# Kernel optimization log

Hardware: AMD Instinct MI355X
Metric: run time of the kernel (lower is better)

Reference implementation:

```python
import jax, jax.numpy as jnp
import numpy as np

N, VW, DW, VP, DP, H, M = 1024, 50000, 300, 50, 100, 512, 256


def _run_dir(x, Wih, Whh, b, reverse):
    # Single-direction LSTM over [n, in] -> [n, H]. PyTorch gate order i,f,g,o.
    Hh = Whh.shape[1]
    def step(carry, xt):
        h, c = carry
        z = xt @ Wih.T + h @ Whh.T + b  # [4H]
        i, f, g, o = jnp.split(z, 4, axis=-1)
        c = jax.nn.sigmoid(f) * c + jax.nn.sigmoid(i) * jnp.tanh(g)
        h = jax.nn.sigmoid(o) * jnp.tanh(c)
        return (h, c), h
    init = (jnp.zeros((Hh,), x.dtype), jnp.zeros((Hh,), x.dtype))
    _, hs = jax.lax.scan(step, init, x, reverse=reverse)
    return hs


def setup_inputs() -> dict:
    key = jax.random.key(0)
    ks = jax.random.split(key, 24)
    s = 0.05  # small init to keep tanh/sigmoid unsaturated
    d = {
        "word_idx": jax.random.randint(ks[0], (N,), 0, VW, dtype=jnp.int32),
        "pos_idx": jax.random.randint(ks[1], (N,), 0, VP, dtype=jnp.int32),
        "word_emb": jax.random.normal(ks[2], (VW, DW), jnp.float32) * s,
        "pos_emb": jax.random.normal(ks[3], (VP, DP), jnp.float32) * s,
        "wih0f": jax.random.normal(ks[4], (4 * H, DW + DP), jnp.float32) * s,
        "whh0f": jax.random.normal(ks[5], (4 * H, H), jnp.float32) * s,
        "b0f": jax.random.normal(ks[6], (4 * H,), jnp.float32) * s,
        "wih0r": jax.random.normal(ks[7], (4 * H, DW + DP), jnp.float32) * s,
        "whh0r": jax.random.normal(ks[8], (4 * H, H), jnp.float32) * s,
        "b0r": jax.random.normal(ks[9], (4 * H,), jnp.float32) * s,
        "wih1f": jax.random.normal(ks[10], (4 * H, 2 * H), jnp.float32) * s,
        "whh1f": jax.random.normal(ks[11], (4 * H, H), jnp.float32) * s,
        "b1f": jax.random.normal(ks[12], (4 * H,), jnp.float32) * s,
        "wih1r": jax.random.normal(ks[13], (4 * H, 2 * H), jnp.float32) * s,
        "whh1r": jax.random.normal(ks[14], (4 * H, H), jnp.float32) * s,
        "b1r": jax.random.normal(ks[15], (4 * H,), jnp.float32) * s,
        "W1": jax.random.normal(ks[16], (M, 4 * H), jnp.float32) * s,
        "bmlp1": jax.random.normal(ks[17], (M,), jnp.float32) * s,
        "w2": jax.random.normal(ks[18], (1, M), jnp.float32) * s,
        "b2": jax.random.normal(ks[19], (1,), jnp.float32) * s,
    }
    return d


def reference(word_idx, pos_idx, word_emb, pos_emb,
              wih0f, whh0f, b0f, wih0r, whh0r, b0r,
              wih1f, whh1f, b1f, wih1r, whh1r, b1r,
              W1, bmlp1, w2, b2):
    # Embed words + pos, concat -> [n, 400]
    x = jnp.concatenate([word_emb[word_idx], pos_emb[pos_idx]], axis=1)
    # 2-layer bidirectional LSTM encoder (batch of 1 squeezed away, as in the module)
    h0 = jnp.concatenate([_run_dir(x, wih0f, whh0f, b0f, False),
                          _run_dir(x, wih0r, whh0r, b0r, True)], axis=1)   # [n, 2H]
    h1 = jnp.concatenate([_run_dir(h0, wih1f, whh1f, b1f, False),
                          _run_dir(h0, wih1r, whh1r, b1r, True)], axis=1)  # [n, 2H]
    # Pairwise MLP score: MLP(concat(h_i, h_j)). Split W1 into head/dep halves so the
    # big GEMM is done once per token instead of once per pair (same math).
    twoH = h1.shape[1]
    a = h1 @ W1[:, :twoH].T            # [n, M], contribution of h_i
    bpart = h1 @ W1[:, twoH:].T        # [n, M], contribution of h_j
    hidden = jnp.tanh(a[:, None, :] + bpart[None, :, :] + bmlp1)  # [n, n, M]
    scores = hidden @ w2[0] + b2[0]    # [n, n]
    return scores
```

## Files before the change

kernel.cpp:

```cpp
#include <hip/hip_runtime.h>
#include <hip/hip_bf16.h>

#define HID   512
#define SEQ   1024
#define GATES 2048

__device__ __forceinline__ float sigm(float x) {
    return 1.f / (1.f + __expf(-x));
}
__device__ __forceinline__ float tanh_fast(float x) {
    float ax = fabsf(x);
    float e  = __expf(-2.f * ax);
    float t  = (1.f - e) * __builtin_amdgcn_rcpf(1.f + e);
    return copysignf(t, x);
}
__device__ __forceinline__ float bcast(float v, int l) {
    return __uint_as_float((unsigned)__builtin_amdgcn_readlane((int)__float_as_uint(v), l));
}

__global__ void embed_kernel(const int* __restrict__ wi, const int* __restrict__ pi,
                             const float* __restrict__ we, const float* __restrict__ pe,
                             float* __restrict__ x) {
    int i = blockIdx.x;
    int t = threadIdx.x;
    const float* w = we + (size_t)wi[i] * 300;
    const float* p = pe + (size_t)pi[i] * 100;
    float* xo = x + (size_t)i * 400;
    for (int c = t; c < 300; c += 128) xo[c]       = w[c];
    for (int c = t; c < 100; c += 128) xo[300 + c] = p[c];
}

__global__ __launch_bounds__(256)
void gemm_bias2(const float* __restrict__ A,
                const float* __restrict__ B0, const float* __restrict__ bias0, float* __restrict__ C0,
                const float* __restrict__ B1, const float* __restrict__ bias1, float* __restrict__ C1,
                int M, int N, int K, int lda, int ldb, int ldc) {
    const float* B    = blockIdx.z ? B1    : B0;
    const float* bias = blockIdx.z ? bias1 : bias0;
    float*       C    = blockIdx.z ? C1    : C0;

    __shared__ __align__(16) float As[16 * 132];
    __shared__ __align__(16) float Bs[16 * 68];
    const int tid  = threadIdx.x;
    const int bn   = blockIdx.x, bm = blockIdx.y;
    const int tj   = tid & 15, ti = tid >> 4;
    const int arow = tid >> 1;
    const int ak8  = (tid & 1) * 8;
    const int brow = tid >> 2;
    const int bk4  = (tid & 3) * 4;
    float acc[8][4] = {};

    for (int kt = 0; kt < K; kt += 16) {
        float4 a0 = *(const float4*)(A + (size_t)(bm * 128 + arow) * lda + kt + ak8);
        float4 a1 = *(const float4*)(A + (size_t)(bm * 128 + arow) * lda + kt + ak8 + 4);
        float4 bv = *(const float4*)(B + (size_t)(bn * 64 + brow) * ldb + kt + bk4);
        As[(ak8 + 0) * 132 + arow] = a0.x; As[(ak8 + 1) * 132 + arow] = a0.y;
        As[(ak8 + 2) * 132 + arow] = a0.z; As[(ak8 + 3) * 132 + arow] = a0.w;
        As[(ak8 + 4) * 132 + arow] = a1.x; As[(ak8 + 5) * 132 + arow] = a1.y;
        As[(ak8 + 6) * 132 + arow] = a1.z; As[(ak8 + 7) * 132 + arow] = a1.w;
        Bs[(bk4 + 0) * 68 + brow] = bv.x; Bs[(bk4 + 1) * 68 + brow] = bv.y;
        Bs[(bk4 + 2) * 68 + brow] = bv.z; Bs[(bk4 + 3) * 68 + brow] = bv.w;
        __syncthreads();
        #pragma unroll
        for (int k = 0; k < 16; ++k) {
            float4 x0 = *(const float4*)&As[k * 132 + ti * 8];
            float4 x1 = *(const float4*)&As[k * 132 + ti * 8 + 4];
            float4 b4 = *(const float4*)&Bs[k * 68 + tj * 4];
            const float av[8] = {x0.x, x0.y, x0.z, x0.w, x1.x, x1.y, x1.z, x1.w};
            #pragma unroll
            for (int i = 0; i < 8; ++i) {
                acc[i][0] = fmaf(av[i], b4.x, acc[i][0]);
                acc[i][1] = fmaf(av[i], b4.y, acc[i][1]);
                acc[i][2] = fmaf(av[i], b4.z, acc[i][2]);
                acc[i][3] = fmaf(av[i], b4.w, acc[i][3]);
            }
        }
        __syncthreads();
    }
    const int n0 = bn * 64 + tj * 4;
    float bb0 = 0.f, bb1 = 0.f, bb2 = 0.f, bb3 = 0.f;
    if (bias) { bb0 = bias[n0]; bb1 = bias[n0 + 1]; bb2 = bias[n0 + 2]; bb3 = bias[n0 + 3]; }
    #pragma unroll
    for (int i = 0; i < 8; ++i) {
        float4 o;
        o.x = acc[i][0] + bb0; o.y = acc[i][1] + bb1;
        o.z = acc[i][2] + bb2; o.w = acc[i][3] + bb3;
        *(float4*)(C + (size_t)(bm * 128 + ti * 8 + i) * ldc + n0) = o;
    }
}

__global__ __launch_bounds__(512)
void lstm_layer(const float* __restrict__ Zf, const float* __restrict__ Zr,
                const float* __restrict__ WhhF, const float* __restrict__ WhhR,
                unsigned long long* __restrict__ Hpair,
                float* __restrict__ Hout,
                unsigned tagBase) {
    const int dir = blockIdx.x >> 5;
    const int wg  = blockIdx.x & 31;
    const float* __restrict__ Z   = dir ? Zr   : Zf;
    const float* __restrict__ Whh = dir ? WhhR : WhhF;
    const int colOff = dir ? HID : 0;

    const int tid  = threadIdx.x;
    const int wave = tid >> 6;
    const int lane = tid & 63;
    const int g    = lane >> 4;
    const int jj   = lane & 15;
    const int grow = g * HID + wg * 16 + jj;

    float w[64];
    {
        const float4* wp = (const float4*)(Whh + (size_t)grow * HID + wave * 64);
        #pragma unroll
        for (int q = 0; q < 16; ++q) {
            float4 v = wp[q];
            w[4 * q] = v.x; w[4 * q + 1] = v.y; w[4 * q + 2] = v.z; w[4 * q + 3] = v.w;
        }
    }

    __shared__ float part[2][8 * 65];
    float cval = 0.f;

    for (int s = 0; s < SEQ; ++s) {
        const int t = dir ? (SEQ - 1 - s) : s;

        float zin = 0.f;
        if (wave == 0) zin = Z[(size_t)t * GATES + grow];

        float acc = 0.f;
        if (s > 0) {
            const int tp = dir ? (t + 1) : (t - 1);
            const unsigned expTag = tagBase + (unsigned)s - 1u;
            const unsigned long long* hp = Hpair + (size_t)tp * (2 * HID) + colOff + wave * 64;
            unsigned long long v;
            for (;;) {
                v = __hip_atomic_load(hp + lane, __ATOMIC_RELAXED, __HIP_MEMORY_SCOPE_AGENT);
                if (__all((unsigned)(v >> 32) == expTag)) break;
            }
            float hv = __uint_as_float((unsigned)v);
            float a0 = 0.f, a1 = 0.f, a2 = 0.f, a3 = 0.f;
            #pragma unroll
            for (int m = 0; m < 64; m += 4) {
                a0 = fmaf(w[m + 0], bcast(hv, m + 0), a0);
                a1 = fmaf(w[m + 1], bcast(hv, m + 1), a1);
                a2 = fmaf(w[m + 2], bcast(hv, m + 2), a2);
                a3 = fmaf(w[m + 3], bcast(hv, m + 3), a3);
            }
            acc = (a0 + a1) + (a2 + a3);
        }
        part[s & 1][wave * 65 + lane] = acc;
        __syncthreads();

        if (wave == 0) {
            const float* pp = part[s & 1];
            float r = zin;
            #pragma unroll
            for (int c = 0; c < 8; ++c) r += pp[c * 65 + lane];
            float nl = (g == 2) ? tanh_fast(r) : sigm(r);
            float ig = __shfl(nl, jj);
            float fg = __shfl(nl, 16 + jj);
            float gg = __shfl(nl, 32 + jj);
            float og = __shfl(nl, 48 + jj);
            if (lane < 16) {
                cval = fg * cval + ig * gg;
                float hv = og * tanh_fast(cval);
                const size_t oidx = (size_t)t * (2 * HID) + colOff + wg * 16 + lane;
                unsigned long long pk = ((unsigned long long)(tagBase + (unsigned)s) << 32)
                                      | (unsigned long long)__float_as_uint(hv);
                __hip_atomic_store(Hpair + oidx, pk, __ATOMIC_RELAXED, __HIP_MEMORY_SCOPE_AGENT);
                Hout[oidx] = hv;
            }
        }
    }
}

__global__ __launch_bounds__(256)
void pairwise_kernel(const float* __restrict__ Ah, const float* __restrict__ Bd,
                     const float* __restrict__ w2, const float* __restrict__ b2,
                     float* __restrict__ out) {
    __shared__ __align__(16) float at[16 * 260];
    __shared__ __align__(16) float bt[16 * 260];
    __shared__ __align__(16) float wl[256];
    const int tid = threadIdx.x;
    const int i0 = blockIdx.y * 16, j0 = blockIdx.x * 16;
    for (int u = tid; u < 16 * 256; u += 256) {
        int r = u >> 8, m = u & 255;
        at[r * 260 + m] = Ah[(size_t)(i0 + r) * 256 + m];
        bt[r * 260 + m] = Bd[(size_t)(j0 + r) * 256 + m];
    }
    wl[tid] = w2[tid];
    __syncthreads();
    const int tj = tid & 15, ti = tid >> 4;
    float acc = b2[0];
    #pragma unroll 2
    for (int m = 0; m < 256; m += 4) {
        float4 a4 = *(const float4*)&at[ti * 260 + m];
        float4 b4 = *(const float4*)&bt[tj * 260 + m];
        float4 w4 = *(const float4*)&wl[m];
        acc += tanh_fast(a4.x + b4.x) * w4.x;
        acc += tanh_fast(a4.y + b4.y) * w4.y;
        acc += tanh_fast(a4.z + b4.z) * w4.z;
        acc += tanh_fast(a4.w + b4.w) * w4.w;
    }
    out[(size_t)(i0 + ti) * 1024 + (j0 + tj)] = acc;
}

extern "C" void kernel_launch(void* const* d_in, const int* in_sizes, int n_in,
                              void* d_out, int out_size, void* d_ws, size_t ws_size,
                              hipStream_t stream) {
    const int*   wi    = (const int*)  d_in[0];
    const int*   pi    = (const int*)  d_in[1];
    const float* we    = (const float*)d_in[2];
    const float* pe    = (const float*)d_in[3];
    const float* wih0f = (const float*)d_in[4];
    const float* whh0f = (const float*)d_in[5];
    const float* b0f   = (const float*)d_in[6];
    const float* wih0r = (const float*)d_in[7];
    const float* whh0r = (const float*)d_in[8];
    const float* b0r   = (const float*)d_in[9];
    const float* wih1f = (const float*)d_in[10];
    const float* whh1f = (const float*)d_in[11];
    const float* b1f   = (const float*)d_in[12];
    const float* wih1r = (const float*)d_in[13];
    const float* whh1r = (const float*)d_in[14];
    const float* b1r   = (const float*)d_in[15];
    const float* W1    = (const float*)d_in[16];
    const float* bmlp1 = (const float*)d_in[17];
    const float* w2    = (const float*)d_in[18];
    const float* b2    = (const float*)d_in[19];
    float* out = (float*)d_out;

    char* wsb = (char*)d_ws;
    float* x  = (float*)(wsb + 512);
    float* zA = x  + (size_t)1024 * 400;
    float* zB = zA + (size_t)1024 * 2048;
    float* h0 = zB + (size_t)1024 * 2048;
    float* h1 = h0 + (size_t)1024 * 1024;
    float* aH = h1 + (size_t)1024 * 1024;
    float* bD = aH + (size_t)1024 * 256;
    unsigned long long* Hpair = (unsigned long long*)(bD + (size_t)1024 * 256);

    embed_kernel<<<dim3(1024), dim3(128), 0, stream>>>(wi, pi, we, pe, x);

    gemm_bias2<<<dim3(32, 8, 2), dim3(256), 0, stream>>>(
        x, wih0f, b0f, zA, wih0r, b0r, zB, 1024, 2048, 400, 400, 400, 2048);

    lstm_layer<<<dim3(64), dim3(512), 0, stream>>>(zA, zB, whh0f, whh0r, Hpair, h0, 1u);

    gemm_bias2<<<dim3(32, 8, 2), dim3(256), 0, stream>>>(
        h0, wih1f, b1f, zA, wih1r, b1r, zB, 1024, 2048, 1024, 1024, 1024, 2048);

    lstm_layer<<<dim3(64), dim3(512), 0, stream>>>(zA, zB, whh1f, whh1r, Hpair, h1, 8192u);

    gemm_bias2<<<dim3(4, 8, 2), dim3(256), 0, stream>>>(
        h1, W1, bmlp1, aH, W1 + 1024, nullptr, bD, 1024, 256, 1024, 1024, 2048, 256);

    pairwise_kernel<<<dim3(64, 64), dim3(256), 0, stream>>>(aH, bD, w2, b2, out);
}
```

Measured before the change: 3.464 ms.

## Specialize LSTM waves into gate wave and matvec waves with Z prefetch

The recurrent LSTM kernel now launches 576 threads per block. Wave 0 only reduces the partial sums, applies the gate nonlinearities and publishes h. The other eight waves hold the Whh slices in registers and do the polled h·Whh matvec. Wave 0 prefetches the next timestep's input-projection row so that global load is off the per-step critical path. The polling loop alternates two outstanding atomic loads to cut spin latency. The cost is one extra wave per block, and correctness now relies on the two roles hitting the same number of barriers per step.

```diff
diff --git a/kernel.cpp b/kernel.cpp
--- a/kernel.cpp
+++ b/kernel.cpp
@@ -89,7 +89,7 @@
     }
 }
 
-__global__ __launch_bounds__(512)
+__global__ __launch_bounds__(576)
 void lstm_layer(const float* __restrict__ Zf, const float* __restrict__ Zr,
                 const float* __restrict__ WhhF, const float* __restrict__ WhhR,
                 unsigned long long* __restrict__ Hpair,
@@ -108,50 +108,19 @@
     const int jj   = lane & 15;
     const int grow = g * HID + wg * 16 + jj;
 
-    float w[64];
-    {
-        const float4* wp = (const float4*)(Whh + (size_t)grow * HID + wave * 64);
-        #pragma unroll
-        for (int q = 0; q < 16; ++q) {
-            float4 v = wp[q];
-            w[4 * q] = v.x; w[4 * q + 1] = v.y; w[4 * q + 2] = v.z; w[4 * q + 3] = v.w;
-        }
-    }
-
     __shared__ float part[2][8 * 65];
-    float cval = 0.f;
-
-    for (int s = 0; s < SEQ; ++s) {
-        const int t = dir ? (SEQ - 1 - s) : s;
-
-        float zin = 0.f;
-        if (wave == 0) zin = Z[(size_t)t * GATES + grow];
-
-        float acc = 0.f;
-        if (s > 0) {
-            const int tp = dir ? (t + 1) : (t - 1);
-            const unsigned expTag = tagBase + (unsigned)s - 1u;
-            const unsigned long long* hp = Hpair + (size_t)tp * (2 * HID) + colOff + wave * 64;
-            unsigned long long v;
-            for (;;) {
-                v = __hip_atomic_load(hp + lane, __ATOMIC_RELAXED, __HIP_MEMORY_SCOPE_AGENT);
-                if (__all((unsigned)(v >> 32) == expTag)) break;
-            }
-            float hv = __uint_as_float((unsigned)v);
-            float a0 = 0.f, a1 = 0.f, a2 = 0.f, a3 = 0.f;
-            #pragma unroll
-            for (int m = 0; m < 64; m += 4) {
-                a0 = fmaf(w[m + 0], bcast(hv, m + 0), a0);
-                a1 = fmaf(w[m + 1], bcast(hv, m + 1), a1);
-                a2 = fmaf(w[m + 2], bcast(hv, m + 2), a2);
-                a3 = fmaf(w[m + 3], bcast(hv, m + 3), a3);
-            }
-            acc = (a0 + a1) + (a2 + a3);
-        }
-        part[s & 1][wave * 65 + lane] = acc;
-        __syncthreads();
-
-        if (wave == 0) {
+
+    if (wave == 0) {
+        float cval = 0.f;
+        float zin = Z[(size_t)(dir ? (SEQ - 1) : 0) * GATES + grow];
+        for (int s = 0; s < SEQ; ++s) {
+            const int t = dir ? (SEQ - 1 - s) : s;
+            float znxt = 0.f;
+            if (s + 1 < SEQ) {
+                const int tn = dir ? (SEQ - 2 - s) : (s + 1);
+                znxt = Z[(size_t)tn * GATES + grow];
+            }
+            __syncthreads();
             const float* pp = part[s & 1];
             float r = zin;
             #pragma unroll
@@ -170,6 +139,48 @@
                 __hip_atomic_store(Hpair + oidx, pk, __ATOMIC_RELAXED, __HIP_MEMORY_SCOPE_AGENT);
                 Hout[oidx] = hv;
             }
+            zin = znxt;
+        }
+    } else {
+        const int kc = wave - 1;
+        float w[64];
+        {
+            const float4* wp = (const float4*)(Whh + (size_t)grow * HID + kc * 64);
+            #pragma unroll
+            for (int q = 0; q < 16; ++q) {
+                float4 v = wp[q];
+                w[4 * q] = v.x; w[4 * q + 1] = v.y; w[4 * q + 2] = v.z; w[4 * q + 3] = v.w;
+            }
+        }
+        for (int s = 0; s < SEQ; ++s) {
+            const int t = dir ? (SEQ - 1 - s) : s;
+            float acc = 0.f;
+            if (s > 0) {
+                const int tp = dir ? (t + 1) : (t - 1);
+                const unsigned expTag = tagBase + (unsigned)s - 1u;
+                const unsigned long long* hp =
+                    Hpair + (size_t)tp * (2 * HID) + colOff + kc * 64 + lane;
+                unsigned long long va, vb, v;
+                va = __hip_atomic_load(hp, __ATOMIC_RELAXED, __HIP_MEMORY_SCOPE_AGENT);
+                for (;;) {
+                    vb = __hip_atomic_load(hp, __ATOMIC_RELAXED, __HIP_MEMORY_SCOPE_AGENT);
+                    if (__all((unsigned)(va >> 32) == expTag)) { v = va; break; }
+                    va = __hip_atomic_load(hp, __ATOMIC_RELAXED, __HIP_MEMORY_SCOPE_AGENT);
+                    if (__all((unsigned)(vb >> 32) == expTag)) { v = vb; break; }
+                }
+                float hv = __uint_as_float((unsigned)v);
+                float a0 = 0.f, a1 = 0.f, a2 = 0.f, a3 = 0.f;
+                #pragma unroll
+                for (int m = 0; m < 64; m += 4) {
+                    a0 = fmaf(w[m + 0], bcast(hv, m + 0), a0);
+                    a1 = fmaf(w[m + 1], bcast(hv, m + 1), a1);
+                    a2 = fmaf(w[m + 2], bcast(hv, m + 2), a2);
+                    a3 = fmaf(w[m + 3], bcast(hv, m + 3), a3);
+                }
+                acc = (a0 + a1) + (a2 + a3);
+            }
+            part[s & 1][kc * 65 + lane] = acc;
+            __syncthreads();
         }
     }
 }
@@ -245,12 +256,12 @@
     gemm_bias2<<<dim3(32, 8, 2), dim3(256), 0, stream>>>(
         x, wih0f, b0f, zA, wih0r, b0r, zB, 1024, 2048, 400, 400, 400, 2048);
 
-    lstm_layer<<<dim3(64), dim3(512), 0, stream>>>(zA, zB, whh0f, whh0r, Hpair, h0, 1u);
+    lstm_layer<<<dim3(64), dim3(576), 0, stream>>>(zA, zB, whh0f, whh0r, Hpair, h0, 1u);
 
     gemm_bias2<<<dim3(32, 8, 2), dim3(256), 0, stream>>>(
         h0, wih1f, b1f, zA, wih1r, b1r, zB, 1024, 2048, 1024, 1024, 1024, 2048);
 
-    lstm_layer<<<dim3(64), dim3(512), 0, stream>>>(zA, zB, whh1f, whh1r, Hpair, h1, 8192u);
+    lstm_layer<<<dim3(64), dim3(576), 0, stream>>>(zA, zB, whh1f, whh1r, Hpair, h1, 8192u);
 
     gemm_bias2<<<dim3(4, 8, 2), dim3(256), 0, stream>>>(
         h1, W1, bmlp1, aH, W1 + 1024, nullptr, bD, 1024, 256, 1024, 1024, 2048, 256);
```

Measured after the change: 3.392 ms. 2.1% less time.
